# Performance work log

Hardware: AMD Instinct MI355X
Metric: run time of the kernel (lower is better)

## Reference

```python
import jax, jax.numpy as jnp
import numpy as np

T, B, C, N, H = 4, 32, 384, 196, 12
D = C // H
HID = 1536
ALPHA = 4.0  # spikingjelly default sigmoid surrogate alpha
EPS = 1e-5   # BatchNorm eps
SCALE = 0.25

@jax.custom_vjp
def spike(x):
    return (x >= 0.0).astype(x.dtype)

def _spike_fwd(x):
    return (x >= 0.0).astype(x.dtype), x

def _spike_bwd(x, g):
    s = jax.nn.sigmoid(ALPHA * x)
    return (g * ALPHA * s * (1.0 - s),)

spike.defvjp(_spike_fwd, _spike_bwd)

def lif(x, thr=1.0, tau=2.0):
    # Multi-step LIF, hard reset to 0, detach_reset=True; x: (T, ...)
    def step(v, xt):
        v = v + (xt - v) / tau
        s = spike(v - thr)
        v = v * (1.0 - jax.lax.stop_gradient(s))
        return v, s
    _, out = jax.lax.scan(step, jnp.zeros_like(x[0]), x)
    return out

def conv_bn(x, w, b, g, beta, m, var):
    # 1x1 Conv1d (= channel matmul) + inference-form BatchNorm1d; x: (T,B,Cin,N), w: (Cout,Cin)
    y = jnp.einsum('tbcn,oc->tbon', x, w)
    if b is not None:
        y = y + b[:, None]
    inv = g * jax.lax.rsqrt(var + EPS)
    return y * inv[:, None] + (beta - m * inv)[:, None]

def _heads(t):
    # (T,B,C,N) -> (T,B,H,N,D), matching transpose(-1,-2).reshape(T,B,N,H,D).permute(0,1,3,2,4)
    return jnp.swapaxes(t, -1, -2).reshape(T, B, N, H, D).transpose(0, 1, 3, 2, 4)

def block_fwd(x, policy, wq, qg, qb, qm, qv, wk, kg, kb, km, kvv, wv, vg, vb, vm, vvv,
              wp, bp, pg, pb, pm, pv, w1, b1, g1, be1, m1, v1, w2, b2, g2, be2, m2, v2):
    q = _heads(lif(conv_bn(x, wq, None, qg, qb, qm, qv)))
    k = _heads(lif(conv_bn(x, wk, None, kg, kb, km, kvv)))
    v = _heads(lif(conv_bn(x, wv, None, vg, vb, vm, vvv)))
    attn = jnp.einsum('tbhnd,tbhmd->tbhnm', q, k)           # (T,B,H,N,N)
    pr = policy.reshape(T, B, 1, 1, N)
    eye = jnp.eye(N, dtype=x.dtype)
    attn = attn * (pr + (1.0 - pr) * eye)                   # attention_policy masking
    o = jnp.einsum('tbhnm,tbhmd->tbhnd', attn, v) * SCALE
    o = jnp.swapaxes(o, 3, 4).reshape(T, B, C, N)           # transpose(3,4).reshape(T,B,C,N)
    o = lif(o, thr=0.5)                                     # attn_lif v_threshold=0.5
    o = lif(conv_bn(o, wp, bp, pg, pb, pm, pv))             # proj conv+bn+lif
    x = x + o                                               # residual 1
    h = lif(conv_bn(x, w1, b1, g1, be1, m1, v1))            # MLP fc1
    h = lif(conv_bn(h, w2, b2, g2, be2, m2, v2))            # MLP fc2
    return x + h                                            # residual 2

def setup_inputs():
    key = jax.random.key(0)
    ks = iter(jax.random.split(key, 48))
    def nrm(shape, s=1.0):
        return jax.random.normal(next(ks), shape, jnp.float32) * s
    def uni(shape):
        return jax.random.uniform(next(ks), shape, jnp.float32, minval=0.5, maxval=1.5)
    inp = {}
    inp['x'] = nrm((T, B, C, N))
    inp['policy'] = (jax.random.uniform(next(ks), (T * B, N, 1)) > 0.3).astype(jnp.float32)
    inp.update({'wq': nrm((C, C), 0.05), 'qg': jnp.ones((C,)), 'qb': jnp.zeros((C,)), 'qm': nrm((C,), 0.1), 'qv': uni((C,))})
    inp.update({'wk': nrm((C, C), 0.05), 'kg': jnp.ones((C,)), 'kb': jnp.zeros((C,)), 'km': nrm((C,), 0.1), 'kvv': uni((C,))})
    inp.update({'wv': nrm((C, C), 0.05), 'vg': jnp.ones((C,)), 'vb': jnp.zeros((C,)), 'vm': nrm((C,), 0.1), 'vvv': uni((C,))})
    inp.update({'wp': nrm((C, C), 0.05), 'bp': jnp.zeros((C,)), 'pg': jnp.ones((C,)), 'pb': jnp.zeros((C,)), 'pm': nrm((C,), 0.1), 'pv': uni((C,))})
    inp.update({'w1': nrm((HID, C), 0.05), 'b1': jnp.zeros((HID,)), 'g1': jnp.ones((HID,)), 'be1': jnp.zeros((HID,)), 'm1': nrm((HID,), 0.1), 'v1': uni((HID,))})
    inp.update({'w2': nrm((C, HID), 0.05), 'b2': jnp.zeros((C,)), 'g2': jnp.ones((C,)), 'be2': jnp.zeros((C,)), 'm2': nrm((C,), 0.1), 'v2': uni((C,))})
    return inp

def reference(x, policy, wq, qg, qb, qm, qv, wk, kg, kb, km, kvv, wv, vg, vb, vm, vvv,
              wp, bp, pg, pb, pm, pv, w1, b1, g1, be1, m1, v1, w2, b2, g2, be2, m2, v2):
    return block_fwd(x, policy, wq, qg, qb, qm, qv, wk, kg, kb, km, kvv, wv, vg, vb, vm, vvv,
                     wp, bp, pg, pb, pm, pv, w1, b1, g1, be1, m1, v1, w2, b2, g2, be2, m2, v2)
```

## Files before the change

### kernel.cpp

```cpp
#include <hip/hip_runtime.h>
#include <cstdint>
#include <cstddef>

#define N_POS 196

typedef __attribute__((ext_vector_type(4))) float f32x4;

__device__ __forceinline__ void async_copy16(const float* g, float* l) {
    __builtin_amdgcn_global_load_lds(
        (const __attribute__((address_space(1))) uint32_t*)g,
        (__attribute__((address_space(3))) uint32_t*)l,
        16, 0, 0);
}

template<int CIN, bool USE_FMA, bool ACCUM>
__global__ __launch_bounds__(256, 4) void convbn_kernel(
    const float* __restrict__ X, const float* __restrict__ W,
    const float* __restrict__ Bi, const float* __restrict__ Ga,
    const float* __restrict__ Be, const float* __restrict__ Mu,
    const float* __restrict__ Va, float* __restrict__ Y, int Cout,
    int nyb, int nb, int b0, int xlocal, int ylocal)
{
#pragma clang fp contract(off)
    constexpr int NCH = CIN / 16;
    __shared__ float lds[2 * 3136 + 64 + 2 * 576];
    float* Xs = lds;
    float* Ws = lds + 6336;
    const int tid = threadIdx.x;
    const int bid = blockIdx.x;
    const int gsz = nyb * 8;
    const int g   = bid / gsz;
    const int rr  = bid - g * gsz;
    const int yblk = rr >> 3;
    const int l   = g * 8 + (rr & 7);
    const int t   = l / nb;
    const int bl  = l - t * nb;
    const int tbg = t * 32 + b0 + bl;
    const int xtb = xlocal ? l : tbg;
    const int ytb = ylocal ? l : tbg;
    const int o0  = yblk * 32;
    const int o   = tid & 31;
    const int grp = tid >> 5;
    const float* Xtb = X + (size_t)xtb * CIN * N_POS;
    const float* Wp  = W + (size_t)o0 * CIN;

    f32x4 accA[4], accB[4];
    #pragma unroll
    for (int i = 0; i < 4; ++i) { accA[i] = (f32x4)0.f; accB[i] = (f32x4)0.f; }

    auto stage = [&](int buf, int kc) {
        const int oo = tid >> 3, k2 = (tid & 7) * 2;
        float2 wv2 = *(const float2*)(Wp + (size_t)oo * CIN + kc + k2);
        #pragma unroll
        for (int j = 0; j < 4; ++j) {
            int i = tid + j * 256;
            if (i < 784)
                async_copy16(Xtb + (size_t)(kc + i / 49) * N_POS + (i % 49) * 4,
                             &Xs[buf * 3136 + (i & ~63) * 4]);
        }
        Ws[buf * 576 + (k2 + 0) * 36 + oo] = wv2.x;
        Ws[buf * 576 + (k2 + 1) * 36 + oo] = wv2.y;
    };

    stage(0, 0);
    __syncthreads();
    int buf = 0;
    for (int ch = 0; ch < NCH; ++ch) {
        if (ch + 1 < NCH) stage(buf ^ 1, (ch + 1) * 16);
        const float* Xb = Xs + buf * 3136 + o * 4;
        const float* Wb = Ws + buf * 576 + grp * 4;
        #pragma unroll
        for (int kk = 0; kk < 16; ++kk) {
            f32x4 xA = *(const f32x4*)(Xb + kk * 196);
            f32x4 xB = *(const f32x4*)(Xb + kk * 196 + 128);
            float4 w4 = *(const float4*)(Wb + kk * 36);
            float w[4] = { w4.x, w4.y, w4.z, w4.w };
            #pragma unroll
            for (int i = 0; i < 4; ++i) {
                f32x4 wd = { w[i], w[i], w[i], w[i] };
                if (USE_FMA) {
                    accA[i] = __builtin_elementwise_fma(wd, xA, accA[i]);
                    accB[i] = __builtin_elementwise_fma(wd, xB, accB[i]);
                } else {
                    accA[i] = accA[i] + wd * xA;
                    accB[i] = accB[i] + wd * xB;
                }
            }
        }
        __syncthreads();
        buf ^= 1;
    }

    #pragma unroll
    for (int i = 0; i < 4; ++i) {
        int oo = o0 + grp * 4 + i;
        float sc = __fmul_rn(Ga[oo], 1.0f / sqrtf(__fadd_rn(Va[oo], 1e-5f)));
        float sh = __fsub_rn(Be[oo], __fmul_rn(Mu[oo], sc));
        float bi = Bi ? Bi[oo] : 0.f;
        float* yp = Y + ((size_t)ytb * Cout + oo) * N_POS;
        {
            float a[4] = { accA[i].x, accA[i].y, accA[i].z, accA[i].w };
            float4 r; float* rp = &r.x;
            #pragma unroll
            for (int j = 0; j < 4; ++j) {
                float y = Bi ? __fadd_rn(a[j], bi) : a[j];
                rp[j] = __fadd_rn(__fmul_rn(y, sc), sh);
            }
            float* dst = yp + o * 4;
            if (ACCUM) {
                float4 y0 = *(const float4*)dst;
                r.x = __fadd_rn(y0.x, r.x); r.y = __fadd_rn(y0.y, r.y);
                r.z = __fadd_rn(y0.z, r.z); r.w = __fadd_rn(y0.w, r.w);
            }
            *(float4*)dst = r;
        }
        if (o <= 16) {
            float a[4] = { accB[i].x, accB[i].y, accB[i].z, accB[i].w };
            float4 r; float* rp = &r.x;
            #pragma unroll
            for (int j = 0; j < 4; ++j) {
                float y = Bi ? __fadd_rn(a[j], bi) : a[j];
                rp[j] = __fadd_rn(__fmul_rn(y, sc), sh);
            }
            float* dst = yp + 128 + o * 4;
            if (ACCUM) {
                float4 y0 = *(const float4*)dst;
                r.x = __fadd_rn(y0.x, r.x); r.y = __fadd_rn(y0.y, r.y);
                r.z = __fadd_rn(y0.z, r.z); r.w = __fadd_rn(y0.w, r.w);
            }
            *(float4*)dst = r;
        }
    }
}

__global__ __launch_bounds__(256) void lif_kernel(float* __restrict__ Y, int plane4, float thr)
{
    int idx = blockIdx.x * 256 + threadIdx.x;
    if (idx >= plane4) return;
    float4* Yp = (float4*)Y;
    float v0 = 0.f, v1 = 0.f, v2 = 0.f, v3 = 0.f;
    #pragma unroll
    for (int t = 0; t < 4; ++t) {
        float4 xv = Yp[(size_t)t * plane4 + idx];
        v0 = __fadd_rn(v0, __fmul_rn(__fsub_rn(xv.x, v0), 0.5f));
        v1 = __fadd_rn(v1, __fmul_rn(__fsub_rn(xv.y, v1), 0.5f));
        v2 = __fadd_rn(v2, __fmul_rn(__fsub_rn(xv.z, v2), 0.5f));
        v3 = __fadd_rn(v3, __fmul_rn(__fsub_rn(xv.w, v3), 0.5f));
        float s0 = (__fsub_rn(v0, thr) >= 0.f) ? 1.f : 0.f;
        float s1 = (__fsub_rn(v1, thr) >= 0.f) ? 1.f : 0.f;
        float s2 = (__fsub_rn(v2, thr) >= 0.f) ? 1.f : 0.f;
        float s3 = (__fsub_rn(v3, thr) >= 0.f) ? 1.f : 0.f;
        v0 = __fmul_rn(v0, 1.f - s0); v1 = __fmul_rn(v1, 1.f - s1);
        v2 = __fmul_rn(v2, 1.f - s2); v3 = __fmul_rn(v3, 1.f - s3);
        xv.x = s0; xv.y = s1; xv.z = s2; xv.w = s3;
        Yp[(size_t)t * plane4 + idx] = xv;
    }
}

__global__ __launch_bounds__(256) void lif_add_kernel(
    const float* __restrict__ Yin, float* __restrict__ Out, int b0)
{
    const int PL4 = 8 * 384 * 49;
    const int B4  = 384 * 49;
    int idx = blockIdx.x * 256 + threadIdx.x;
    if (idx >= PL4) return;
    int bl = idx / B4, r = idx - bl * B4;
    const float4* Yp = (const float4*)Yin;
    float v0 = 0.f, v1 = 0.f, v2 = 0.f, v3 = 0.f;
    #pragma unroll
    for (int t = 0; t < 4; ++t) {
        float4 xv = Yp[(size_t)t * PL4 + idx];
        v0 = __fadd_rn(v0, __fmul_rn(__fsub_rn(xv.x, v0), 0.5f));
        v1 = __fadd_rn(v1, __fmul_rn(__fsub_rn(xv.y, v1), 0.5f));
        v2 = __fadd_rn(v2, __fmul_rn(__fsub_rn(xv.z, v2), 0.5f));
        v3 = __fadd_rn(v3, __fmul_rn(__fsub_rn(xv.w, v3), 0.5f));
        float s0 = (__fsub_rn(v0, 1.0f) >= 0.f) ? 1.f : 0.f;
        float s1 = (__fsub_rn(v1, 1.0f) >= 0.f) ? 1.f : 0.f;
        float s2 = (__fsub_rn(v2, 1.0f) >= 0.f) ? 1.f : 0.f;
        float s3 = (__fsub_rn(v3, 1.0f) >= 0.f) ? 1.f : 0.f;
        v0 = __fmul_rn(v0, 1.f - s0); v1 = __fmul_rn(v1, 1.f - s1);
        v2 = __fmul_rn(v2, 1.f - s2); v3 = __fmul_rn(v3, 1.f - s3);
        float4* op = (float4*)Out + ((size_t)(t * 32 + b0 + bl) * B4 + r);
        float4 o = *op;
        o.x = __fadd_rn(o.x, s0); o.y = __fadd_rn(o.y, s1);
        o.z = __fadd_rn(o.z, s2); o.w = __fadd_rn(o.w, s3);
        *op = o;
    }
}

__global__ __launch_bounds__(256) void pack_kernel(const float* __restrict__ S,
                                                   uint32_t* __restrict__ Bits)
{
    int idx = blockIdx.x * 256 + threadIdx.x;
    if (idx >= 4 * 32 * 12 * 196) return;
    int n = idx % 196;
    int rest = idx / 196;
    int h = rest % 12;
    int tb = rest / 12;
    const float* sp = S + ((size_t)tb * 384 + h * 32) * 196 + n;
    uint32_t bits = 0;
    #pragma unroll
    for (int d = 0; d < 32; ++d)
        bits |= (sp[(size_t)d * 196] > 0.5f) ? (1u << d) : 0u;
    Bits[idx] = bits;
}

__global__ __launch_bounds__(256) void attn_kernel(
    const uint32_t* __restrict__ Qb, const uint32_t* __restrict__ Kb,
    const float* __restrict__ V, const float* __restrict__ P, float* __restrict__ O)
{
    __shared__ uint32_t Qbs[196], Kbs[196];
    __shared__ float Ps[196];
    __shared__ float Vs[32][204];
    __shared__ float Ss[32][204];
    __shared__ float Os[32][36];
    const int tid = threadIdx.x;
    const int bid = blockIdx.x;
    const int tb = bid / 12, h = bid - tb * 12;
    const size_t vbase = ((size_t)tb * 384 + h * 32) * 196;
    const size_t qbase = ((size_t)tb * 12 + h) * 196;
    for (int i = tid; i < 196; i += 256) {
        Qbs[i] = Qb[qbase + i];
        Kbs[i] = Kb[qbase + i];
        Ps[i]  = P[(size_t)tb * 196 + i];
    }
    for (int i = tid; i < 32 * 49; i += 256) {
        int d = i / 49, m4 = i - d * 49;
        *(float4*)&Vs[d][m4 * 4] = *(const float4*)(V + vbase + (size_t)d * 196 + m4 * 4);
    }
    __syncthreads();
    for (int n0 = 0; n0 < 196; n0 += 32) {
        const int rows = min(32, 196 - n0);
        for (int idx = tid; idx < rows * 196; idx += 256) {
            int ns = idx / 196, m = idx - ns * 196;
            int n = n0 + ns;
            float s = (float)__popc(Qbs[n] & Kbs[m]);
            float p = Ps[m];
            float e = (m == n) ? 1.f : 0.f;
            Ss[ns][m] = s * (p + (1.f - p) * e);
        }
        __syncthreads();
        {
            const int tn = tid & 15, td = tid >> 4;
            float a00 = 0, a01 = 0, a10 = 0, a11 = 0;
            #pragma unroll 7
            for (int m4 = 0; m4 < 49; ++m4) {
                float4 s0 = *(const float4*)&Ss[tn][m4 * 4];
                float4 s1 = *(const float4*)&Ss[tn + 16][m4 * 4];
                float4 u0 = *(const float4*)&Vs[td][m4 * 4];
                float4 u1 = *(const float4*)&Vs[td + 16][m4 * 4];
                a00 += s0.x * u0.x + s0.y * u0.y + s0.z * u0.z + s0.w * u0.w;
                a01 += s0.x * u1.x + s0.y * u1.y + s0.z * u1.z + s0.w * u1.w;
                a10 += s1.x * u0.x + s1.y * u0.y + s1.z * u0.z + s1.w * u0.w;
                a11 += s1.x * u1.x + s1.y * u1.y + s1.z * u1.z + s1.w * u1.w;
            }
            Os[td     ][tn     ] = a00 * 0.25f;
            Os[td + 16][tn     ] = a01 * 0.25f;
            Os[td     ][tn + 16] = a10 * 0.25f;
            Os[td + 16][tn + 16] = a11 * 0.25f;
        }
        __syncthreads();
        {
            const int d = tid >> 3, c4 = tid & 7;
            if (c4 * 4 < rows)
                *(float4*)(O + vbase + (size_t)d * 196 + n0 + c4 * 4) =
                    *(const float4*)&Os[d][c4 * 4];
        }
        __syncthreads();
    }
}

__global__ __launch_bounds__(256) void add_kernel(const float* __restrict__ A,
    const float* __restrict__ B, float* __restrict__ Out, int n4)
{
    int idx = blockIdx.x * 256 + threadIdx.x;
    if (idx >= n4) return;
    float4 a = ((const float4*)A)[idx];
    float4 b = ((const float4*)B)[idx];
    float4 o;
    o.x = __fadd_rn(a.x, b.x); o.y = __fadd_rn(a.y, b.y);
    o.z = __fadd_rn(a.z, b.z); o.w = __fadd_rn(a.w, b.w);
    ((float4*)Out)[idx] = o;
}

extern "C" void kernel_launch(void* const* d_in, const int* in_sizes, int n_in,
                              void* d_out, int out_size, void* d_ws, size_t ws_size,
                              hipStream_t stream) {
    const float* x   = (const float*)d_in[0];
    const float* pol = (const float*)d_in[1];
    const float* wq = (const float*)d_in[2];
    const float* qg = (const float*)d_in[3];
    const float* qb = (const float*)d_in[4];
    const float* qm = (const float*)d_in[5];
    const float* qv = (const float*)d_in[6];
    const float* wk = (const float*)d_in[7];
    const float* kg = (const float*)d_in[8];
    const float* kb = (const float*)d_in[9];
    const float* km = (const float*)d_in[10];
    const float* kvv= (const float*)d_in[11];
    const float* wv = (const float*)d_in[12];
    const float* vg = (const float*)d_in[13];
    const float* vb = (const float*)d_in[14];
    const float* vm = (const float*)d_in[15];
    const float* vvv= (const float*)d_in[16];
    const float* wp = (const float*)d_in[17];
    const float* bp = (const float*)d_in[18];
    const float* pg = (const float*)d_in[19];
    const float* pb = (const float*)d_in[20];
    const float* pm = (const float*)d_in[21];
    const float* pv = (const float*)d_in[22];
    const float* w1 = (const float*)d_in[23];
    const float* b1 = (const float*)d_in[24];
    const float* g1 = (const float*)d_in[25];
    const float* be1= (const float*)d_in[26];
    const float* m1 = (const float*)d_in[27];
    const float* v1 = (const float*)d_in[28];
    const float* w2 = (const float*)d_in[29];
    const float* b2 = (const float*)d_in[30];
    const float* g2 = (const float*)d_in[31];
    const float* be2= (const float*)d_in[32];
    const float* m2 = (const float*)d_in[33];
    const float* v2 = (const float*)d_in[34];

    float* bufA = (float*)d_ws;
    float* bufD = bufA + 9633792;
    uint32_t* Qbits = (uint32_t*)(bufD + 2408448);
    uint32_t* Kbits = Qbits + 301056;
    float* out = (float*)d_out;

    convbn_kernel<384, false, false><<<1536, 256, 0, stream>>>(x, wq, nullptr, qg, qb, qm, qv, bufA, 384, 12, 32, 0, 0, 0);
    lif_kernel<<<2352, 256, 0, stream>>>(bufA, 602112, 1.0f);
    pack_kernel<<<1176, 256, 0, stream>>>(bufA, Qbits);
    convbn_kernel<384, false, false><<<1536, 256, 0, stream>>>(x, wk, nullptr, kg, kb, km, kvv, bufA, 384, 12, 32, 0, 0, 0);
    lif_kernel<<<2352, 256, 0, stream>>>(bufA, 602112, 1.0f);
    pack_kernel<<<1176, 256, 0, stream>>>(bufA, Kbits);
    convbn_kernel<384, false, false><<<1536, 256, 0, stream>>>(x, wv, nullptr, vg, vb, vm, vvv, bufA, 384, 12, 32, 0, 0, 0);
    lif_kernel<<<2352, 256, 0, stream>>>(bufA, 602112, 1.0f);

    attn_kernel<<<1536, 256, 0, stream>>>(Qbits, Kbits, bufA, pol, out);
    lif_kernel<<<2352, 256, 0, stream>>>(out, 602112, 0.5f);

    convbn_kernel<384, true, false><<<1536, 256, 0, stream>>>(out, wp, bp, pg, pb, pm, pv, bufA, 384, 12, 32, 0, 0, 0);
    lif_kernel<<<2352, 256, 0, stream>>>(bufA, 602112, 1.0f);
    add_kernel<<<9408, 256, 0, stream>>>(x, bufA, out, 2408448);

    for (int c = 0; c < 4; ++c) {
        convbn_kernel<384, false, false><<<1536, 256, 0, stream>>>(out, w1, b1, g1, be1, m1, v1, bufA, 1536, 48, 8, c * 8, 0, 1);
        lif_kernel<<<2352, 256, 0, stream>>>(bufA, 602112, 1.0f);
        convbn_kernel<1536, true, false><<<384, 256, 0, stream>>>(bufA, w2, b2, g2, be2, m2, v2, bufD, 384, 12, 8, c * 8, 1, 1);
        lif_add_kernel<<<588, 256, 0, stream>>>(bufD, out, c * 8);
    }
}
```

Before: 2.477 ms.

## Fuse Q/K/V 1x1 conv+BN into one kernel sharing staged input tiles

Adds a convqkv kernel that computes the Q, K and V channel matmuls plus BatchNorm in one pass. Each input tile is staged into LDS once and reused against all three weight sets. This removes two of the three reads of x and two kernel launches. It uses three separate output buffers, so it needs a larger workspace and falls back to the old path when the workspace is too small. Three sets of accumulators raise register pressure, and the launch bound drops to 3 blocks per CU.

New measurement: 2.478 ms. No clear change (+0.1%).

```diff
diff --git a/kernel.cpp b/kernel.cpp
--- a/kernel.cpp
+++ b/kernel.cpp
@@ -129,6 +129,135 @@
                 r.z = __fadd_rn(y0.z, r.z); r.w = __fadd_rn(y0.w, r.w);
             }
             *(float4*)dst = r;
+        }
+    }
+}
+
+__global__ __launch_bounds__(256, 3) void convqkv_kernel(
+    const float* __restrict__ X,
+    const float* __restrict__ Wq, const float* __restrict__ Wk, const float* __restrict__ Wv,
+    const float* __restrict__ QG, const float* __restrict__ QB,
+    const float* __restrict__ QM, const float* __restrict__ QV,
+    const float* __restrict__ KG, const float* __restrict__ KB,
+    const float* __restrict__ KM, const float* __restrict__ KVv,
+    const float* __restrict__ VG, const float* __restrict__ VB,
+    const float* __restrict__ VM, const float* __restrict__ VVv,
+    float* __restrict__ Yq, float* __restrict__ Yk, float* __restrict__ Yv)
+{
+#pragma clang fp contract(off)
+    __shared__ float lds[2 * 3136 + 64 + 3 * 2 * 576];
+    float* Xs  = lds;
+    float* Wqs = lds + 6336;
+    float* Wks = Wqs + 1152;
+    float* Wvs = Wks + 1152;
+    const int tid = threadIdx.x;
+    const int bid = blockIdx.x;
+    const int g   = bid / 96;
+    const int rr  = bid - g * 96;
+    const int yblk = rr >> 3;
+    const int tb  = g * 8 + (rr & 7);
+    const int o0  = yblk * 32;
+    const int o   = tid & 31;
+    const int grp = tid >> 5;
+    const float* Xtb = X + (size_t)tb * 384 * N_POS;
+
+    f32x4 aQA[4], aQB[4], aKA[4], aKB[4], aVA[4], aVB[4];
+    #pragma unroll
+    for (int i = 0; i < 4; ++i) {
+        aQA[i] = (f32x4)0.f; aQB[i] = (f32x4)0.f;
+        aKA[i] = (f32x4)0.f; aKB[i] = (f32x4)0.f;
+        aVA[i] = (f32x4)0.f; aVB[i] = (f32x4)0.f;
+    }
+
+    auto stage = [&](int buf, int kc) {
+        const int oo = tid >> 3, k2 = (tid & 7) * 2;
+        const size_t woff = (size_t)(o0 + oo) * 384 + kc + k2;
+        float2 wq2 = *(const float2*)(Wq + woff);
+        float2 wk2 = *(const float2*)(Wk + woff);
+        float2 wv2 = *(const float2*)(Wv + woff);
+        #pragma unroll
+        for (int j = 0; j < 4; ++j) {
+            int i = tid + j * 256;
+            if (i < 784)
+                async_copy16(Xtb + (size_t)(kc + i / 49) * N_POS + (i % 49) * 4,
+                             &Xs[buf * 3136 + (i & ~63) * 4]);
+        }
+        Wqs[buf * 576 + (k2 + 0) * 36 + oo] = wq2.x;
+        Wqs[buf * 576 + (k2 + 1) * 36 + oo] = wq2.y;
+        Wks[buf * 576 + (k2 + 0) * 36 + oo] = wk2.x;
+        Wks[buf * 576 + (k2 + 1) * 36 + oo] = wk2.y;
+        Wvs[buf * 576 + (k2 + 0) * 36 + oo] = wv2.x;
+        Wvs[buf * 576 + (k2 + 1) * 36 + oo] = wv2.y;
+    };
+
+    stage(0, 0);
+    __syncthreads();
+    int buf = 0;
+    for (int ch = 0; ch < 24; ++ch) {
+        if (ch + 1 < 24) stage(buf ^ 1, (ch + 1) * 16);
+        const float* Xb  = Xs  + buf * 3136 + o * 4;
+        const float* Wqb = Wqs + buf * 576 + grp * 4;
+        const float* Wkb = Wks + buf * 576 + grp * 4;
+        const float* Wvb = Wvs + buf * 576 + grp * 4;
+        #pragma unroll
+        for (int kk = 0; kk < 16; ++kk) {
+            f32x4 xA = *(const f32x4*)(Xb + kk * 196);
+            f32x4 xB = *(const f32x4*)(Xb + kk * 196 + 128);
+            float4 q4 = *(const float4*)(Wqb + kk * 36);
+            float4 k4 = *(const float4*)(Wkb + kk * 36);
+            float4 v4 = *(const float4*)(Wvb + kk * 36);
+            float qw[4] = { q4.x, q4.y, q4.z, q4.w };
+            float kw[4] = { k4.x, k4.y, k4.z, k4.w };
+            float vw[4] = { v4.x, v4.y, v4.z, v4.w };
+            #pragma unroll
+            for (int i = 0; i < 4; ++i) {
+                f32x4 wd;
+                wd = (f32x4){ qw[i], qw[i], qw[i], qw[i] };
+                aQA[i] = aQA[i] + wd * xA;  aQB[i] = aQB[i] + wd * xB;
+                wd = (f32x4){ kw[i], kw[i], kw[i], kw[i] };
+                aKA[i] = aKA[i] + wd * xA;  aKB[i] = aKB[i] + wd * xB;
+                wd = (f32x4){ vw[i], vw[i], vw[i], vw[i] };
+                aVA[i] = aVA[i] + wd * xA;  aVB[i] = aVB[i] + wd * xB;
+            }
+        }
+        __syncthreads();
+        buf ^= 1;
+    }
+
+    const size_t ybase = (size_t)tb * 384;
+    #pragma unroll
+    for (int br = 0; br < 3; ++br) {
+        const f32x4* aA = (br == 0) ? aQA : (br == 1) ? aKA : aVA;
+        const f32x4* aB = (br == 0) ? aQB : (br == 1) ? aKB : aVB;
+        const float* G  = (br == 0) ? QG : (br == 1) ? KG : VG;
+        const float* Bt = (br == 0) ? QB : (br == 1) ? KB : VB;
+        const float* M  = (br == 0) ? QM : (br == 1) ? KM : VM;
+        const float* Va = (br == 0) ? QV : (br == 1) ? KVv : VVv;
+        float* Y        = (br == 0) ? Yq : (br == 1) ? Yk : Yv;
+        #pragma unroll
+        for (int i = 0; i < 4; ++i) {
+            int oo = o0 + grp * 4 + i;
+            float sc = __fmul_rn(G[oo], 1.0f / sqrtf(__fadd_rn(Va[oo], 1e-5f)));
+            float sh = __fsub_rn(Bt[oo], __fmul_rn(M[oo], sc));
+            float* yp = Y + (ybase + oo) * N_POS;
+            {
+                float a[4] = { aA[i].x, aA[i].y, aA[i].z, aA[i].w };
+                float4 r;
+                r.x = __fadd_rn(__fmul_rn(a[0], sc), sh);
+                r.y = __fadd_rn(__fmul_rn(a[1], sc), sh);
+                r.z = __fadd_rn(__fmul_rn(a[2], sc), sh);
+                r.w = __fadd_rn(__fmul_rn(a[3], sc), sh);
+                *(float4*)(yp + o * 4) = r;
+            }
+            if (o <= 16) {
+                float a[4] = { aB[i].x, aB[i].y, aB[i].z, aB[i].w };
+                float4 r;
+                r.x = __fadd_rn(__fmul_rn(a[0], sc), sh);
+                r.y = __fadd_rn(__fmul_rn(a[1], sc), sh);
+                r.z = __fadd_rn(__fmul_rn(a[2], sc), sh);
+                r.w = __fadd_rn(__fmul_rn(a[3], sc), sh);
+                *(float4*)(yp + 128 + o * 4) = r;
+            }
         }
     }
 }
@@ -321,33 +450,66 @@
     const float* be2= (const float*)d_in[32];
     const float* m2 = (const float*)d_in[33];
     const float* v2 = (const float*)d_in[34];
-
-    float* bufA = (float*)d_ws;
-    float* bufD = bufA + 9633792;
-    uint32_t* Qbits = (uint32_t*)(bufD + 2408448);
-    uint32_t* Kbits = Qbits + 301056;
     float* out = (float*)d_out;
 
-    convbn_kernel<384, false, false><<<1536, 256, 0, stream>>>(x, wq, nullptr, qg, qb, qm, qv, bufA, 384, 12, 32, 0, 0, 0);
-    lif_kernel<<<2352, 256, 0, stream>>>(bufA, 602112, 1.0f);
-    pack_kernel<<<1176, 256, 0, stream>>>(bufA, Qbits);
-    convbn_kernel<384, false, false><<<1536, 256, 0, stream>>>(x, wk, nullptr, kg, kb, km, kvv, bufA, 384, 12, 32, 0, 0, 0);
-    lif_kernel<<<2352, 256, 0, stream>>>(bufA, 602112, 1.0f);
-    pack_kernel<<<1176, 256, 0, stream>>>(bufA, Kbits);
-    convbn_kernel<384, false, false><<<1536, 256, 0, stream>>>(x, wv, nullptr, vg, vb, vm, vvv, bufA, 384, 12, 32, 0, 0, 0);
-    lif_kernel<<<2352, 256, 0, stream>>>(bufA, 602112, 1.0f);
-
-    attn_kernel<<<1536, 256, 0, stream>>>(Qbits, Kbits, bufA, pol, out);
-    lif_kernel<<<2352, 256, 0, stream>>>(out, 602112, 0.5f);
-
-    convbn_kernel<384, true, false><<<1536, 256, 0, stream>>>(out, wp, bp, pg, pb, pm, pv, bufA, 384, 12, 32, 0, 0, 0);
-    lif_kernel<<<2352, 256, 0, stream>>>(bufA, 602112, 1.0f);
-    add_kernel<<<9408, 256, 0, stream>>>(x, bufA, out, 2408448);
-
-    for (int c = 0; c < 4; ++c) {
-        convbn_kernel<384, false, false><<<1536, 256, 0, stream>>>(out, w1, b1, g1, be1, m1, v1, bufA, 1536, 48, 8, c * 8, 0, 1);
+    const bool fused = ws_size >= (size_t)31911936 * 4;
+
+    if (fused) {
+        float* bufV = (float*)d_ws;
+        float* bufQ = bufV + 9633792;
+        float* bufK = bufQ + 9633792;
+        float* bufD = bufK + 9633792;
+        uint32_t* Qbits = (uint32_t*)(bufD + 2408448);
+        uint32_t* Kbits = Qbits + 301056;
+
+        convqkv_kernel<<<1536, 256, 0, stream>>>(x, wq, wk, wv,
+            qg, qb, qm, qv, kg, kb, km, kvv, vg, vb, vm, vvv, bufQ, bufK, bufV);
+        lif_kernel<<<2352, 256, 0, stream>>>(bufQ, 602112, 1.0f);
+        pack_kernel<<<1176, 256, 0, stream>>>(bufQ, Qbits);
+        lif_kernel<<<2352, 256, 0, stream>>>(bufK, 602112, 1.0f);
+        pack_kernel<<<1176, 256, 0, stream>>>(bufK, Kbits);
+        lif_kernel<<<2352, 256, 0, stream>>>(bufV, 602112, 1.0f);
+
+        attn_kernel<<<1536, 256, 0, stream>>>(Qbits, Kbits, bufV, pol, out);
+        lif_kernel<<<2352, 256, 0, stream>>>(out, 602112, 0.5f);
+
+        convbn_kernel<384, true, false><<<1536, 256, 0, stream>>>(out, wp, bp, pg, pb, pm, pv, bufQ, 384, 12, 32, 0, 0, 0);
+        lif_kernel<<<2352, 256, 0, stream>>>(bufQ, 602112, 1.0f);
+        add_kernel<<<9408, 256, 0, stream>>>(x, bufQ, out, 2408448);
+
+        for (int c = 0; c < 4; ++c) {
+            convbn_kernel<384, false, false><<<1536, 256, 0, stream>>>(out, w1, b1, g1, be1, m1, v1, bufQ, 1536, 48, 8, c * 8, 0, 1);
+            lif_kernel<<<2352, 256, 0, stream>>>(bufQ, 602112, 1.0f);
+            convbn_kernel<1536, true, false><<<384, 256, 0, stream>>>(bufQ, w2, b2, g2, be2, m2, v2, bufD, 384, 12, 8, c * 8, 1, 1);
+            lif_add_kernel<<<588, 256, 0, stream>>>(bufD, out, c * 8);
+        }
+    } else {
+        float* bufA = (float*)d_ws;
+        float* bufD = bufA + 9633792;
+        uint32_t* Qbits = (uint32_t*)(bufD + 2408448);
+        uint32_t* Kbits = Qbits + 301056;
+
+        convbn_kernel<384, false, false><<<1536, 256, 0, stream>>>(x, wq, nullptr, qg, qb, qm, qv, bufA, 384, 12, 32, 0, 0, 0);
         lif_kernel<<<2352, 256, 0, stream>>>(bufA, 602112, 1.0f);
-        convbn_kernel<1536, true, false><<<384, 256, 0, stream>>>(bufA, w2, b2, g2, be2, m2, v2, bufD, 384, 12, 8, c * 8, 1, 1);
-        lif_add_kernel<<<588, 256, 0, stream>>>(bufD, out, c * 8);
-    }
-}
+        pack_kernel<<<1176, 256, 0, stream>>>(bufA, Qbits);
+        convbn_kernel<384, false, false><<<1536, 256, 0, stream>>>(x, wk, nullptr, kg, kb, km, kvv, bufA, 384, 12, 32, 0, 0, 0);
+        lif_kernel<<<2352, 256, 0, stream>>>(bufA, 602112, 1.0f);
+        pack_kernel<<<1176, 256, 0, stream>>>(bufA, Kbits);
+        convbn_kernel<384, false, false><<<1536, 256, 0, stream>>>(x, wv, nullptr, vg, vb, vm, vvv, bufA, 384, 12, 32, 0, 0, 0);
+        lif_kernel<<<2352, 256, 0, stream>>>(bufA, 602112, 1.0f);
+
+        attn_kernel<<<1536, 256, 0, stream>>>(Qbits, Kbits, bufA, pol, out);
+        lif_kernel<<<2352, 256, 0, stream>>>(out, 602112, 0.5f);
+
+        convbn_kernel<384, true, false><<<1536, 256, 0, stream>>>(out, wp, bp, pg, pb, pm, pv, bufA, 384, 12, 32, 0, 0, 0);
+        lif_kernel<<<2352, 256, 0, stream>>>(bufA, 602112, 1.0f);
+        add_kernel<<<9408, 256, 0, stream>>>(x, bufA, out, 2408448);
+
+        for (int c = 0; c < 4; ++c) {
+            convbn_kernel<384, false, false><<<1536, 256, 0, stream>>>(out, w1, b1, g1, be1, m1, v1, bufA, 1536, 48, 8, c * 8, 0, 1);
+            lif_kernel<<<2352, 256, 0, stream>>>(bufA, 602112, 1.0f);
+            convbn_kernel<1536, true, false><<<384, 256, 0, stream>>>(bufA, w2, b2, g2, be2, m2, v2, bufD, 384, 12, 8, c * 8, 1, 1);
+            lif_add_kernel<<<588, 256, 0, stream>>>(bufD, out, c * 8);
+        }
+    }
+}
```
